# Kernel optimization log

Measured on AMD Instinct MI355X. Metric: run time of the kernel, lower is better.

The kernel has to match this reference:

```python
import jax, jax.numpy as jnp
import numpy as np

B, N, IN_F = 8, 1024, 512
H, D = 4, 128  # num_heads, out_features; H*D == IN_F for residual
LN_EPS = 1e-5
NEG_INF = -1e9


def setup_inputs() -> dict:
    key = jax.random.key(0)
    ks = jax.random.split(key, 7)
    x = jax.random.normal(ks[0], (B, N, IN_F), dtype=jnp.float32)
    mask = jax.random.randint(ks[1], (B, N), 0, 2, dtype=jnp.int32)
    # xavier-uniform-ish init scales
    W = jax.random.uniform(ks[2], (IN_F, H * D), dtype=jnp.float32, minval=-1.0, maxval=1.0) * (1.414 * np.sqrt(6.0 / (IN_F + H * D)))
    a_src = jax.random.uniform(ks[3], (H, D), dtype=jnp.float32, minval=-1.0, maxval=1.0) * (1.414 * np.sqrt(6.0 / (H + D)))
    a_dst = jax.random.uniform(ks[4], (H, D), dtype=jnp.float32, minval=-1.0, maxval=1.0) * (1.414 * np.sqrt(6.0 / (H + D)))
    gamma = jnp.ones((H * D,), dtype=jnp.float32)
    beta = jnp.zeros((H * D,), dtype=jnp.float32)
    return {"x": x, "mask": mask, "W": W, "a_src": a_src, "a_dst": a_dst, "gamma": gamma, "beta": beta}


def _layernorm(y, gamma, beta):
    mu = jnp.mean(y, axis=-1, keepdims=True)
    var = jnp.var(y, axis=-1, keepdims=True)
    return (y - mu) * jax.lax.rsqrt(var + LN_EPS) * gamma + beta


def reference(x, mask, W, a_src, a_dst, gamma, beta):
    b, n, _ = x.shape
    h = (x @ W).reshape(b, n, H, D)                      # [B,N,H,D]
    e_i = jnp.einsum('bnhd,hd->bnh', h, a_src)           # [B,N,H]
    e_j = jnp.einsum('bnhd,hd->bnh', h, a_dst)           # [B,N,H]
    e = jax.nn.leaky_relu(e_i[:, :, None, :] + e_j[:, None, :, :], 0.2)  # [B,N,N,H]
    mm = mask[:, None, :, None] * mask[:, :, None, None]  # [B,N,N,1]
    e = jnp.where(mm == 0, NEG_INF, e)
    attn = jax.nn.softmax(e, axis=2)                     # softmax over neighbors j
    h_prime = jnp.einsum('bnjh,bjhd->bnhd', attn, h).reshape(b, n, H * D)
    return _layernorm(h_prime + x, gamma, beta)
```

## Files before the change

kernel.cpp:

```cpp
#include <hip/hip_runtime.h>
#include <math.h>

#define Bsz 8
#define Nn 1024
#define Ff 512
#define Hh 4
#define Dd 128

typedef float f32x4 __attribute__((ext_vector_type(4)));
typedef short bf16x8 __attribute__((ext_vector_type(8)));

#define LOG2E 1.44269504f

__device__ inline uint f2b1(float a) {
    union { float f; uint u; } v; v.f = a;
    return (v.u + 0x7fffu + ((v.u >> 16) & 1u)) >> 16;
}
__device__ inline uint f2b_pk(float a, float b) { return f2b1(a) | (f2b1(b) << 16); }


__global__ __launch_bounds__(256) void conv_w(const float* __restrict__ Wm,
                                              ushort* __restrict__ Wc) {
    __shared__ float tile[8 * 520];
    const int kb = blockIdx.x, tid = threadIdx.x;
    const int l = tid & 63, wv = tid >> 6;
    const int col0 = l * 8;
    #pragma unroll
    for (int rsel = 0; rsel < 2; ++rsel) {
        int kr = wv + rsel * 4;
        const float4* wp = (const float4*)(Wm + (size_t)(kb * 8 + kr) * Ff + col0);
        float4 a = wp[0], c = wp[1];
        *(float4*)(&tile[kr * 520 + col0]) = a;
        *(float4*)(&tile[kr * 520 + col0 + 4]) = c;
    }
    __syncthreads();
    #pragma unroll
    for (int rsel = 0; rsel < 2; ++rsel) {
        int n = tid + rsel * 256;
        float v[8];
        #pragma unroll
        for (int u = 0; u < 8; ++u) v[u] = tile[u * 520 + n];
        uint4 o = { f2b_pk(v[0], v[1]), f2b_pk(v[2], v[3]),
                    f2b_pk(v[4], v[5]), f2b_pk(v[6], v[7]) };
        int nc = n >> 7, nt = (n >> 4) & 7, n15 = n & 15;
        *(uint4*)(Wc + ((size_t)(((nc * 64 + kb) * 8 + nt) * 16 + n15) << 3)) = o;
    }
}

__global__ __launch_bounds__(256, 2) void gemm_xw(const float* __restrict__ X,
                                                  const ushort* __restrict__ Wc,
                                                  const float* __restrict__ a_src,
                                                  const float* __restrict__ a_dst,
                                                  ushort* __restrict__ hT,
                                                  float* __restrict__ ei,
                                                  float* __restrict__ ej) {
    const int idx = blockIdx.x;
    const int b = idx & 7, sub = idx >> 3;
    const int mi = sub & 15, nc = sub >> 4;
    const int tid = threadIdx.x;
    const int w = tid >> 6, lane = tid & 63, quad = lane >> 4, l16 = lane & 15;
    const int mtile = (b * 16 + mi) * 4 + w;

    f32x4 z = {0.f, 0.f, 0.f, 0.f};
    f32x4 acc[8];
    #pragma unroll
    for (int nt = 0; nt < 8; ++nt) acc[nt] = z;

    const float* ap = X + (size_t)(mtile * 16 + l16) * Ff + quad * 8;
    const ushort* bp = Wc + ((size_t)nc << 16) + quad * 1024 + l16 * 8;

#define LOADA(s, dst) { \
        float4 f0_ = *(const float4*)(ap + (s) * 32); \
        float4 f1_ = *(const float4*)(ap + (s) * 32 + 4); \
        union { uint4 u; bf16x8 v; } o_; \
        o_.u.x = f2b_pk(f0_.x, f0_.y); o_.u.y = f2b_pk(f0_.z, f0_.w); \
        o_.u.z = f2b_pk(f1_.x, f1_.y); o_.u.w = f2b_pk(f1_.z, f1_.w); \
        dst = o_.v; }

    bf16x8 ab[2];
    bf16x8 bb[2][8];
    LOADA(0, ab[0]);
    LOADA(1, ab[1]);
    #pragma unroll
    for (int nt = 0; nt < 8; ++nt) {
        bb[0][nt] = *(const bf16x8*)(bp + nt * 128);
        bb[1][nt] = *(const bf16x8*)(bp + 4096 + nt * 128);
    }

    #pragma unroll 2
    for (int s = 0; s < 16; ++s) {
        const int c = s & 1;
        #pragma unroll
        for (int nt = 0; nt < 8; ++nt)
            acc[nt] = __builtin_amdgcn_mfma_f32_16x16x32_bf16(ab[c], bb[c][nt], acc[nt], 0, 0, 0);
        if (s + 2 < 16) {
            LOADA(s + 2, ab[c]);
            #pragma unroll
            for (int nt = 0; nt < 8; ++nt)
                bb[c][nt] = *(const bf16x8*)(bp + (s + 2) * 4096 + nt * 128);
        }
    }
#undef LOADA

    const int nseq = (mi * 4 + w) * 16 + quad * 4;
    const int jb = nseq >> 5, js = nseq & 31;
    #pragma unroll
    for (int nt = 0; nt < 8; ++nt) {
        uint2 pv;
        pv.x = f2b_pk(acc[nt][0], acc[nt][1]);
        pv.y = f2b_pk(acc[nt][2], acc[nt][3]);
        int hd = nc * 128 + nt * 16 + l16;
        *(uint2*)(hT + ((size_t)(b * 32 + jb)) * 16384 + (size_t)hd * 32 + js) = pv;
    }

    {
        float as4[8], ad4[8];
        #pragma unroll
        for (int nt = 0; nt < 8; ++nt) {
            as4[nt] = a_src[nc * 128 + nt * 16 + l16] * LOG2E;
            ad4[nt] = a_dst[nc * 128 + nt * 16 + l16] * LOG2E;
        }
        #pragma unroll
        for (int rr = 0; rr < 4; ++rr) {
            float v1 = 0.f, v2 = 0.f;
            #pragma unroll
            for (int nt = 0; nt < 8; ++nt) {
                v1 += acc[nt][rr] * as4[nt];
                v2 += acc[nt][rr] * ad4[nt];
            }
            #pragma unroll
            for (int off = 1; off < 16; off <<= 1) {
                v1 += __shfl_xor(v1, off);
                v2 += __shfl_xor(v2, off);
            }
            if (l16 == 0) {
                int n = nseq + rr;
                ei[((b * 4 + nc) << 10) + n] = v1;
                ej[((b * 4 + nc) << 10) + n] = v2;
            }
        }
    }
}

__global__ __launch_bounds__(512, 2) void attn_pv(const ushort* __restrict__ hT,
                                                  const float* __restrict__ ei_g,
                                                  const float* __restrict__ ej_g,
                                                  const int* __restrict__ mask,
                                                  const float* __restrict__ X,
                                                  const float* __restrict__ gamma,
                                                  const float* __restrict__ beta,
                                                  float* __restrict__ out) {
    __shared__ float s_ep[32 * 516];
    __shared__ float s_as[4][32];

    const int idx = blockIdx.x;
    const int b = idx & 7, i0 = (idx >> 3) * 32;
    const int tid = threadIdx.x;
    const int w = tid >> 6, w4 = w & 3, jh = w >> 2;
    const int lane = tid & 63, quad = lane >> 4, l16 = lane & 15;

    const float* ejh = ej_g + ((b * 4 + w4) << 10);
    const int* mkb = mask + (b << 10);

    float maxej = -3.0e38f;
    #pragma unroll
    for (int k = 0; k < 16; ++k) maxej = fmaxf(maxej, ejh[lane + 64 * k]);
    #pragma unroll
    for (int off = 1; off < 64; off <<= 1) maxej = fmaxf(maxej, __shfl_xor(maxej, off));

    const float ei0 = ei_g[((b * 4 + w4) << 10) + i0 + l16];
    const float ei1 = ei_g[((b * 4 + w4) << 10) + i0 + 16 + l16];
    const int mi0 = mkb[i0 + l16];
    const int mi1 = mkb[i0 + 16 + l16];
    float m0, m1;
    { float t = ei0 + maxej; m0 = mi0 ? fmaxf(t, 0.2f * t) : -1e9f; }
    { float t = ei1 + maxej; m1 = mi1 ? fmaxf(t, 0.2f * t) : -1e9f; }

    f32x4 z = {0.f, 0.f, 0.f, 0.f};
    f32x4 acc[2][8], asum[2];
    #pragma unroll
    for (int it = 0; it < 2; ++it) { asum[it] = z;
        #pragma unroll
        for (int dt = 0; dt < 8; ++dt) acc[it][dt] = z; }
    bf16x8 ones;
    #pragma unroll
    for (int q = 0; q < 8; ++q) ones[q] = (short)0x3F80;

    const ushort* hTb = hT + ((size_t)(b * 32)) * 16384 + (size_t)(w4 * 128) * 32
                        + l16 * 32 + quad * 8;

    bf16x8 B[2][8];
    #pragma unroll
    for (int c = 0; c < 2; ++c) {
        const ushort* h0 = hTb + (size_t)(jh * 16 + c) * 16384;
        #pragma unroll
        for (int dt = 0; dt < 8; ++dt) B[c][dt] = *(const bf16x8*)(h0 + dt * 512);
    }

    #pragma unroll 2
    for (int r = 0; r < 16; ++r) {
        const int c = r & 1;
        const int jq = (jh * 16 + r) * 32 + quad * 8;
        float4 e0 = *(const float4*)(ejh + jq);
        float4 e1 = *(const float4*)(ejh + jq + 4);
        int4 q0 = *(const int4*)(mkb + jq);
        int4 q1 = *(const int4*)(mkb + jq + 4);
        float ev[8] = {e0.x, e0.y, e0.z, e0.w, e1.x, e1.y, e1.z, e1.w};
        int   mv[8] = {q0.x, q0.y, q0.z, q0.w, q1.x, q1.y, q1.z, q1.w};
        float wv0[8], wv1[8];
        #pragma unroll
        for (int u = 0; u < 8; ++u) {
            float t0 = ei0 + ev[u];
            float l0 = fmaxf(t0, 0.2f * t0);
            wv0[u] = __builtin_amdgcn_exp2f(((mi0 && mv[u]) ? l0 : -1e9f) - m0);
            float t1 = ei1 + ev[u];
            float l1 = fmaxf(t1, 0.2f * t1);
            wv1[u] = __builtin_amdgcn_exp2f(((mi1 && mv[u]) ? l1 : -1e9f) - m1);
        }
        union { uint4 u; bf16x8 v; } af0, af1;
        af0.u.x = f2b_pk(wv0[0], wv0[1]); af0.u.y = f2b_pk(wv0[2], wv0[3]);
        af0.u.z = f2b_pk(wv0[4], wv0[5]); af0.u.w = f2b_pk(wv0[6], wv0[7]);
        af1.u.x = f2b_pk(wv1[0], wv1[1]); af1.u.y = f2b_pk(wv1[2], wv1[3]);
        af1.u.z = f2b_pk(wv1[4], wv1[5]); af1.u.w = f2b_pk(wv1[6], wv1[7]);
        asum[0] = __builtin_amdgcn_mfma_f32_16x16x32_bf16(af0.v, ones, asum[0], 0, 0, 0);
        asum[1] = __builtin_amdgcn_mfma_f32_16x16x32_bf16(af1.v, ones, asum[1], 0, 0, 0);
        #pragma unroll
        for (int dt = 0; dt < 8; ++dt) {
            acc[0][dt] = __builtin_amdgcn_mfma_f32_16x16x32_bf16(af0.v, B[c][dt], acc[0][dt], 0, 0, 0);
            acc[1][dt] = __builtin_amdgcn_mfma_f32_16x16x32_bf16(af1.v, B[c][dt], acc[1][dt], 0, 0, 0);
        }
        if (r + 2 < 16) {
            const ushort* hn = hTb + (size_t)(jh * 16 + r + 2) * 16384;
            #pragma unroll
            for (int dt = 0; dt < 8; ++dt) B[c][dt] = *(const bf16x8*)(hn + dt * 512);
        }
    }

    if (jh == 1) {
        #pragma unroll
        for (int it = 0; it < 2; ++it)
            #pragma unroll
            for (int dt = 0; dt < 8; ++dt)
                #pragma unroll
                for (int rr = 0; rr < 4; ++rr)
                    s_ep[(it * 16 + quad * 4 + rr) * 516 + w4 * 128 + dt * 16 + l16] =
                        acc[it][dt][rr];
        if (l16 == 0) {
            #pragma unroll
            for (int it = 0; it < 2; ++it)
                #pragma unroll
                for (int rr = 0; rr < 4; ++rr)
                    s_as[w4][it * 16 + quad * 4 + rr] = asum[it][rr];
        }
    }
    __syncthreads();
    if (jh == 0) {
        float rs[2][4];
        #pragma unroll
        for (int it = 0; it < 2; ++it)
            #pragma unroll
            for (int rr = 0; rr < 4; ++rr)
                rs[it][rr] = 1.f / (asum[it][rr] + s_as[w4][it * 16 + quad * 4 + rr]);
        #pragma unroll
        for (int it = 0; it < 2; ++it)
            #pragma unroll
            for (int dt = 0; dt < 8; ++dt)
                #pragma unroll
                for (int rr = 0; rr < 4; ++rr) {
                    int off = (it * 16 + quad * 4 + rr) * 516 + w4 * 128 + dt * 16 + l16;
                    s_ep[off] = (acc[it][dt][rr] + s_ep[off]) * rs[it][rr];
                }
    }
    __syncthreads();

    #pragma unroll
    for (int q = 0; q < 4; ++q) {
        int ir = w * 4 + q;
        int ig = i0 + ir;
        float4 p0 = *(const float4*)(&s_ep[ir * 516 + lane * 8]);
        float4 p1 = *(const float4*)(&s_ep[ir * 516 + lane * 8 + 4]);
        const float* xp = X + (((size_t)((b << 10) + ig)) << 9) + lane * 8;
        float4 x0 = *(const float4*)(xp);
        float4 x1 = *(const float4*)(xp + 4);
        float v[8] = {p0.x + x0.x, p0.y + x0.y, p0.z + x0.z, p0.w + x0.w,
                      p1.x + x1.x, p1.y + x1.y, p1.z + x1.z, p1.w + x1.w};
        float s1 = 0.f, s2 = 0.f;
        #pragma unroll
        for (int u = 0; u < 8; ++u) { s1 += v[u]; s2 += v[u] * v[u]; }
        #pragma unroll
        for (int off = 1; off < 64; off <<= 1) { s1 += __shfl_xor(s1, off); s2 += __shfl_xor(s2, off); }
        float mean = s1 * (1.f / 512.f);
        float var  = s2 * (1.f / 512.f) - mean * mean;
        float rstd = rsqrtf(var + 1e-5f);
        int f0i = lane * 8;
        float4 g0 = *(const float4*)(gamma + f0i);
        float4 g1 = *(const float4*)(gamma + f0i + 4);
        float4 be0 = *(const float4*)(beta + f0i);
        float4 be1 = *(const float4*)(beta + f0i + 4);
        float* op = out + (((size_t)((b << 10) + ig)) << 9) + f0i;
        float4 o0, o1;
        o0.x = (v[0] - mean) * rstd * g0.x + be0.x;
        o0.y = (v[1] - mean) * rstd * g0.y + be0.y;
        o0.z = (v[2] - mean) * rstd * g0.z + be0.z;
        o0.w = (v[3] - mean) * rstd * g0.w + be0.w;
        o1.x = (v[4] - mean) * rstd * g1.x + be1.x;
        o1.y = (v[5] - mean) * rstd * g1.y + be1.y;
        o1.z = (v[6] - mean) * rstd * g1.z + be1.z;
        o1.w = (v[7] - mean) * rstd * g1.w + be1.w;
        *(float4*)op = o0;
        *(float4*)(op + 4) = o1;
    }
}

extern "C" void kernel_launch(void* const* d_in, const int* in_sizes, int n_in,
                              void* d_out, int out_size, void* d_ws, size_t ws_size,
                              hipStream_t stream) {
    const float* x     = (const float*)d_in[0];
    const int*   mask  = (const int*)d_in[1];
    const float* W     = (const float*)d_in[2];
    const float* a_src = (const float*)d_in[3];
    const float* a_dst = (const float*)d_in[4];
    const float* gamma = (const float*)d_in[5];
    const float* beta  = (const float*)d_in[6];
    float* out = (float*)d_out;

    ushort* hT = (ushort*)d_ws;
    ushort* Wc = hT + (size_t)8 * 512 * 1024;
    float* ei = (float*)(Wc + (size_t)512 * 512);
    float* ej = ei + 32768;

    conv_w<<<dim3(64), 256, 0, stream>>>(W, Wc);
    gemm_xw<<<dim3(512), 256, 0, stream>>>(x, Wc, a_src, a_dst, hT, ei, ej);
    attn_pv<<<dim3(256), 512, 0, stream>>>(hT, ei, ej, mask, x, gamma, beta, out);
}
```

Measured before the change: 125.4 us.

## Stage W tiles in double-buffered shared memory shared across waves in gemm_xw

Instead of every wave loading its own copy of the W tile from global memory into registers, the block cooperatively loads each 4096-element W k-slice once into a double-buffered LDS array and each wave reads its B fragments from LDS. This cuts redundant global/L2 traffic (4 waves previously fetched the same W data) and reduces register pressure from the bb[2][8] array. It adds a __syncthreads per k-step and LDS read latency in the MFMA loop.

```diff
diff --git a/kernel.cpp b/kernel.cpp
--- a/kernel.cpp
+++ b/kernel.cpp
@@ -54,6 +54,7 @@
                                                   ushort* __restrict__ hT,
                                                   float* __restrict__ ei,
                                                   float* __restrict__ ej) {
+    __shared__ ushort Bs[2][4096];
     const int idx = blockIdx.x;
     const int b = idx & 7, sub = idx >> 3;
     const int mi = sub & 15, nc = sub >> 4;
@@ -67,7 +68,8 @@
     for (int nt = 0; nt < 8; ++nt) acc[nt] = z;
 
     const float* ap = X + (size_t)(mtile * 16 + l16) * Ff + quad * 8;
-    const ushort* bp = Wc + ((size_t)nc << 16) + quad * 1024 + l16 * 8;
+    const ushort* wsrc = Wc + ((size_t)nc << 16) + tid * 16;
+    const int brd = quad * 1024 + l16 * 8;
 
 #define LOADA(s, dst) { \
         float4 f0_ = *(const float4*)(ap + (s) * 32); \
@@ -78,27 +80,34 @@
         dst = o_.v; }
 
     bf16x8 ab[2];
-    bf16x8 bb[2][8];
+    bf16x8 br0, br1;
+
     LOADA(0, ab[0]);
     LOADA(1, ab[1]);
-    #pragma unroll
-    for (int nt = 0; nt < 8; ++nt) {
-        bb[0][nt] = *(const bf16x8*)(bp + nt * 128);
-        bb[1][nt] = *(const bf16x8*)(bp + 4096 + nt * 128);
-    }
+    br0 = *(const bf16x8*)(wsrc);
+    br1 = *(const bf16x8*)(wsrc + 8);
+    *(bf16x8*)(&Bs[0][tid * 16]) = br0;
+    *(bf16x8*)(&Bs[0][tid * 16 + 8]) = br1;
+    __syncthreads();
 
     #pragma unroll 2
     for (int s = 0; s < 16; ++s) {
         const int c = s & 1;
-        #pragma unroll
-        for (int nt = 0; nt < 8; ++nt)
-            acc[nt] = __builtin_amdgcn_mfma_f32_16x16x32_bf16(ab[c], bb[c][nt], acc[nt], 0, 0, 0);
-        if (s + 2 < 16) {
-            LOADA(s + 2, ab[c]);
-            #pragma unroll
-            for (int nt = 0; nt < 8; ++nt)
-                bb[c][nt] = *(const bf16x8*)(bp + (s + 2) * 4096 + nt * 128);
-        }
+        if (s + 1 < 16) {
+            br0 = *(const bf16x8*)(wsrc + (s + 1) * 4096);
+            br1 = *(const bf16x8*)(wsrc + (s + 1) * 4096 + 8);
+        }
+        #pragma unroll
+        for (int nt = 0; nt < 8; ++nt) {
+            bf16x8 bf = *(const bf16x8*)(&Bs[c][brd + nt * 128]);
+            acc[nt] = __builtin_amdgcn_mfma_f32_16x16x32_bf16(ab[c], bf, acc[nt], 0, 0, 0);
+        }
+        if (s + 2 < 16) LOADA(s + 2, ab[c]);
+        if (s + 1 < 16) {
+            *(bf16x8*)(&Bs[(s + 1) & 1][tid * 16]) = br0;
+            *(bf16x8*)(&Bs[(s + 1) & 1][tid * 16 + 8]) = br1;
+        }
+        __syncthreads();
     }
 #undef LOADA
 
```

New measurement: 124.9 us. Within noise of the previous version (-0.4%).
